# Kernel optimization log

Hardware: AMD Instinct MI355X
Metric: run time of the kernel (lower is better)

Reference implementation:

```python
import jax, jax.numpy as jnp
import numpy as np

B, L, D, H = 32768, 11, 32, 4
HD = D // H
VOCAB, NPOS, PE = 10000, 16, 16
EPS = 1e-5


def _safe_mask(m):
    # disable padding mask for rows where ALL positions are padding
    all_pad = m.all(axis=1)
    return m & ~all_pad[:, None]


def _aggregate(out, query_mask):
    sm = _safe_mask(query_mask)
    valid = (~sm)[..., None].astype(out.dtype)  # (B, L, 1)
    return (out * valid).sum(axis=1) / jnp.clip(valid.sum(axis=1), 1.0, None)


def _mha(xq, xkv, in_w, in_b, out_w, out_b, kpm):
    # torch nn.MultiheadAttention (batch_first, eval): packed in_proj then out_proj
    Bq, Lq, _ = xq.shape
    Wq, Wk, Wv = jnp.split(in_w, 3, axis=0)
    bq, bk, bv = jnp.split(in_b, 3, axis=0)
    q = (xq @ Wq.T + bq).reshape(Bq, Lq, H, HD)
    k = (xkv @ Wk.T + bk).reshape(Bq, -1, H, HD)
    v = (xkv @ Wv.T + bv).reshape(Bq, -1, H, HD)
    s = jnp.einsum('bqhd,bkhd->bhqk', q, k) / np.sqrt(HD).astype(np.float32)
    s = jnp.where(kpm[:, None, None, :], -jnp.inf, s)
    a = jax.nn.softmax(s, axis=-1)
    o = jnp.einsum('bhqk,bkhd->bqhd', a, v).reshape(Bq, Lq, D)
    return o @ out_w.T + out_b


def setup_inputs() -> dict:
    key = jax.random.key(0)
    ks = jax.random.split(key, 14)
    inp = {
        'home_players': jax.random.randint(ks[0], (B, L), 0, VOCAB),
        'away_players': jax.random.randint(ks[1], (B, L), 0, VOCAB),
        'h_positions': jax.random.randint(ks[2], (B, L), 0, NPOS),
        'a_positions': jax.random.randint(ks[3], (B, L), 0, NPOS),
        'emb': jax.random.normal(ks[4], (VOCAB, PE), jnp.float32) * 0.02,
        'pos_emb': jax.random.normal(ks[5], (NPOS, PE), jnp.float32) * 0.02,
        'h2a_in_w': jax.random.normal(ks[6], (3 * D, D), jnp.float32) * 0.05,
        'h2a_in_b': jnp.zeros((3 * D,), jnp.float32),
        'h2a_out_w': jax.random.normal(ks[7], (D, D), jnp.float32) * 0.05,
        'h2a_out_b': jnp.zeros((D,), jnp.float32),
        'a2h_in_w': jax.random.normal(ks[8], (3 * D, D), jnp.float32) * 0.05,
        'a2h_in_b': jnp.zeros((3 * D,), jnp.float32),
        'a2h_out_w': jax.random.normal(ks[9], (D, D), jnp.float32) * 0.05,
        'a2h_out_b': jnp.zeros((D,), jnp.float32),
        'gate_w': jax.random.normal(ks[10], (D, 2 * D), jnp.float32) * 0.05,
        'gate_b': jnp.zeros((D,), jnp.float32),
        'ln_w': jnp.ones((D,), jnp.float32),
        'ln_b': jnp.zeros((D,), jnp.float32),
    }
    return inp


def reference(home_players, away_players, h_positions, a_positions,
              emb, pos_emb,
              h2a_in_w, h2a_in_b, h2a_out_w, h2a_out_b,
              a2h_in_w, a2h_in_b, a2h_out_w, a2h_out_b,
              gate_w, gate_b, ln_w, ln_b):
    h_vecs = jnp.concatenate([emb[home_players], pos_emb[h_positions]], axis=-1)  # (B,L,D)
    a_vecs = jnp.concatenate([emb[away_players], pos_emb[a_positions]], axis=-1)
    h_mask = home_players == 0
    a_mask = away_players == 0
    h2a_out = _mha(h_vecs, a_vecs, h2a_in_w, h2a_in_b, h2a_out_w, h2a_out_b, _safe_mask(a_mask))
    h2a_vec = _aggregate(h2a_out, h_mask)
    a2h_out = _mha(a_vecs, h_vecs, a2h_in_w, a2h_in_b, a2h_out_w, a2h_out_b, _safe_mask(h_mask))
    a2h_vec = _aggregate(a2h_out, a_mask)
    concat = jnp.concatenate([h2a_vec, a2h_vec], axis=1)
    gate = jax.nn.sigmoid(concat @ gate_w.T + gate_b)
    matchup = gate * h2a_vec + (1.0 - gate) * a2h_vec
    mu = matchup.mean(axis=-1, keepdims=True)
    var = ((matchup - mu) ** 2).mean(axis=-1, keepdims=True)
    return (matchup - mu) / jnp.sqrt(var + EPS) * ln_w + ln_b
```

## Files before the change

### kernel.cpp

```cpp
#include <hip/hip_runtime.h>
#include <hip/hip_bf16.h>

typedef unsigned int u32;
typedef unsigned short u16;
typedef short bf16x8 __attribute__((ext_vector_type(8)));
typedef float f32x4 __attribute__((ext_vector_type(4)));

#define LQ 11
#define RPB 8
#define NR 88
#define PSTR 40
#define XSTR 32

__device__ __forceinline__ float blo(u32 x) { return __uint_as_float(x << 16); }
__device__ __forceinline__ float bhi(u32 x) { return __uint_as_float(x & 0xFFFF0000u); }
__device__ __forceinline__ float bf1(u16 x) { return __uint_as_float(((u32)x) << 16); }
__device__ __forceinline__ u16 f2b(float f) {
    __hip_bfloat16 h = __float2bfloat16(f);
    return *reinterpret_cast<u16*>(&h);
}
__device__ __forceinline__ u32 pk2(float a, float b) {
    return (u32)f2b(a) | ((u32)f2b(b) << 16);
}

__global__ __launch_bounds__(512, 6)
void CrossTeam_v7(const int* __restrict__ home, const int* __restrict__ away,
                  const int* __restrict__ hpos, const int* __restrict__ apos,
                  const float* __restrict__ emb, const float* __restrict__ pemb,
                  const float* __restrict__ h2a_w, const float* __restrict__ h2a_b,
                  const float* __restrict__ h2a_ow, const float* __restrict__ h2a_ob,
                  const float* __restrict__ a2h_w, const float* __restrict__ a2h_b,
                  const float* __restrict__ a2h_ow, const float* __restrict__ a2h_ob,
                  const float* __restrict__ gw, const float* __restrict__ gb,
                  const float* __restrict__ lnw, const float* __restrict__ lnb,
                  float* __restrict__ out)
{
    __shared__ u16 proj[6][NR * PSTR];
    __shared__ union {
        u16 xst[2][NR * XSTR];
        struct {
            float obuf[2][RPB][32];
            float ybuf[2][RPB][32];
        } cd;
    } u;
    __shared__ u32 mraw[2][RPB];

    const int t = threadIdx.x;
    const int b0 = blockIdx.x * RPB;

    if (t < 192) {
        const int side = t / 96;
        const int s = t - side * 96;
        if (s < NR) {
            const int r = s / 11, l = s - r * 11;
            const int gi = (b0 + r) * LQ + l;
            const int pid = side ? away[gi] : home[gi];
            const int pp  = side ? apos[gi] : hpos[gi];
            const f32x4* er = (const f32x4*)(emb + pid * 16);
            const f32x4* pr = (const f32x4*)(pemb + pp * 16);
            const f32x4 e0 = er[0], e1 = er[1], e2 = er[2], e3 = er[3];
            const f32x4 p0 = pr[0], p1 = pr[1], p2 = pr[2], p3 = pr[3];
            uint4 q0, q1, q2, q3;
            q0.x = pk2(e0[0], e0[1]); q0.y = pk2(e0[2], e0[3]);
            q0.z = pk2(e1[0], e1[1]); q0.w = pk2(e1[2], e1[3]);
            q1.x = pk2(e2[0], e2[1]); q1.y = pk2(e2[2], e2[3]);
            q1.z = pk2(e3[0], e3[1]); q1.w = pk2(e3[2], e3[3]);
            q2.x = pk2(p0[0], p0[1]); q2.y = pk2(p0[2], p0[3]);
            q2.z = pk2(p1[0], p1[1]); q2.w = pk2(p1[2], p1[3]);
            q3.x = pk2(p2[0], p2[1]); q3.y = pk2(p2[2], p2[3]);
            q3.z = pk2(p3[0], p3[1]); q3.w = pk2(p3[2], p3[3]);
            uint4* dst = (uint4*)&u.xst[side][s * XSTR];
            const int sw = s & 3;
            dst[0 ^ sw] = q0; dst[1 ^ sw] = q1; dst[2 ^ sw] = q2; dst[3 ^ sw] = q3;
        }
    }
    if (t >= 496) {
        const int k = t - 496; const int side = k >> 3; const int r = k & 7;
        const int* arr = side ? away : home;
        u32 m = 0;
        for (int l = 0; l < LQ; ++l) m |= (u32)(arr[(b0 + r) * LQ + l] == 0) << l;
        mraw[side][r] = m;
    }
    __syncthreads();

    const int wave = t >> 6, lane = t & 63;
    const int lq = lane >> 4, lm = lane & 15;

    {
        const int side = wave >> 2;
        const int mh = (wave >> 1) & 1;
        const int nh = wave & 1;
        const float* wq_src  = side ? a2h_w : h2a_w;
        const float* wkv_src = side ? h2a_w : a2h_w;
        const float* bq_src  = side ? a2h_b : h2a_b;
        const float* bkv_src = side ? h2a_b : a2h_b;
        bf16x8 afrag[3]; float bias[3][4];
        #pragma unroll
        for (int i = 0; i < 3; ++i) {
            const int M = (mh * 3 + i) * 16;
            const float* ws = (M < 32) ? wq_src : wkv_src;
            const float* wp = ws + (M + lm) * 32 + lq * 8;
            const f32x4 a0 = *(const f32x4*)wp;
            const f32x4 a1 = *(const f32x4*)(wp + 4);
            union { bf16x8 v; u32 w[4]; } au;
            au.w[0] = pk2(a0[0], a0[1]); au.w[1] = pk2(a0[2], a0[3]);
            au.w[2] = pk2(a1[0], a1[1]); au.w[3] = pk2(a1[2], a1[3]);
            afrag[i] = au.v;
            const float* bs = (M < 32) ? bq_src : bkv_src;
            #pragma unroll
            for (int j = 0; j < 4; ++j) bias[i][j] = bs[M + lq * 4 + j];
        }
        #pragma unroll
        for (int nn = 0; nn < 3; ++nn) {
            const int n = nh * 3 + nn;
            const int row = n * 16 + lm;
            const int rrow = row < NR ? row : NR - 1;
            const bf16x8 bfrag = *(const bf16x8*)
                &u.xst[side][rrow * XSTR + ((lq ^ (rrow & 3)) * 8)];
            #pragma unroll
            for (int i = 0; i < 3; ++i) {
                f32x4 acc = { bias[i][0], bias[i][1], bias[i][2], bias[i][3] };
                acc = __builtin_amdgcn_mfma_f32_16x16x32_bf16(afrag[i], bfrag, acc, 0, 0, 0);
                const int mt = mh * 3 + i;
                const int mat = side * 3 + (mt >> 1);
                const int dimw = (mt & 1) * 16 + lq * 4;
                if (row < NR) {
                    uint2 pk;
                    pk.x = pk2(acc[0], acc[1]);
                    pk.y = pk2(acc[2], acc[3]);
                    *(uint2*)&proj[mat][row * PSTR + dimw] = pk;
                }
            }
        }
    }
    __syncthreads();

    {
        const int hh = lane >> 4;
        const int slot = lane & 15;
        const int qi = slot < 11 ? slot : 10;
        const int dpv = hh * 8 + (slot & 7);
        #pragma unroll
        for (int it = 0; it < 2; ++it) {
            const int task = wave * 2 + it;
            const int r = task >> 1, dir = task & 1;
            const int qmat = dir ? 3 : 0;
            const int kmat = dir ? 1 : 4;
            const int vmat = dir ? 2 : 5;
            const u32 kvraw = mraw[dir ? 0 : 1][r];
            const u32 kv = (kvraw == 0x7FFu) ? 0u : kvraw;
            const u32 qraw = mraw[dir ? 1 : 0][r];
            const u32 smq = (qraw == 0x7FFu) ? 0u : qraw;
            const u32 vm = (~smq) & 0x7FFu;
            const float invc = 1.0f / (float)__popc(vm);
            const float wqw = (slot < 11 && ((vm >> slot) & 1u)) ? invc : 0.f;
            const uint4 qp = *(const uint4*)&proj[qmat][(r * 11 + qi) * PSTR + hh * 8];
            float qv[8];
            qv[0]=blo(qp.x); qv[1]=bhi(qp.x); qv[2]=blo(qp.y); qv[3]=bhi(qp.y);
            qv[4]=blo(qp.z); qv[5]=bhi(qp.z); qv[6]=blo(qp.w); qv[7]=bhi(qp.w);
            float e[11]; float sum = 0.f;
            #pragma unroll
            for (int ki = 0; ki < 11; ++ki) {
                const uint4 kp = *(const uint4*)&proj[kmat][(r * 11 + ki) * PSTR + hh * 8];
                float s = qv[0]*blo(kp.x) + qv[1]*bhi(kp.x) + qv[2]*blo(kp.y) + qv[3]*bhi(kp.y)
                        + qv[4]*blo(kp.z) + qv[5]*bhi(kp.z) + qv[6]*blo(kp.w) + qv[7]*bhi(kp.w);
                s *= 0.35355339059327373f;
                e[ki] = ((kv >> ki) & 1u) ? 0.f : __expf(s);
                sum += e[ki];
            }
            const float rs = wqw / fmaxf(sum, 1e-20f);
            float o = 0.f;
            #pragma unroll
            for (int ki = 0; ki < 11; ++ki) {
                float v = e[ki] * rs;
                v += __shfl_xor(v, 1, 16);
                v += __shfl_xor(v, 2, 16);
                v += __shfl_xor(v, 4, 16);
                v += __shfl_xor(v, 8, 16);
                o += v * bf1(proj[vmat][(r * 11 + ki) * PSTR + dpv]);
            }
            if (slot < 8) u.cd.obuf[dir][r][dpv] = o;
        }
    }
    __syncthreads();

    if (t < 256) {
        const int r = t >> 5, d = t & 31;
        float yh = h2a_ob[d];
        const float* wr = h2a_ow + d * 32;
        #pragma unroll
        for (int c = 0; c < 32; ++c) yh += u.cd.obuf[0][r][c] * wr[c];
        float ya = a2h_ob[d];
        wr = a2h_ow + d * 32;
        #pragma unroll
        for (int c = 0; c < 32; ++c) ya += u.cd.obuf[1][r][c] * wr[c];
        u.cd.ybuf[0][r][d] = yh; u.cd.ybuf[1][r][d] = ya;
        float acc = gb[d];
        const float* gr = gw + d * 64;
        #pragma unroll
        for (int c = 0; c < 32; ++c) acc += u.cd.ybuf[0][r][c] * gr[c];
        #pragma unroll
        for (int c = 0; c < 32; ++c) acc += u.cd.ybuf[1][r][c] * gr[32 + c];
        const float g = 1.0f / (1.0f + __expf(-acc));
        const float m = g * yh + (1.0f - g) * ya;
        float s1 = m, s2 = m * m;
        #pragma unroll
        for (int off = 1; off < 32; off <<= 1) {
            s1 += __shfl_xor(s1, off, 32);
            s2 += __shfl_xor(s2, off, 32);
        }
        const float mu = s1 * 0.03125f;
        const float var = fmaxf(s2 * 0.03125f - mu * mu, 0.f);
        const float res = (m - mu) * rsqrtf(var + 1e-5f) * lnw[d] + lnb[d];
        out[(b0 + r) * 32 + d] = res;
    }
}

extern "C" void kernel_launch(void* const* d_in, const int* in_sizes, int n_in,
                              void* d_out, int out_size, void* d_ws, size_t ws_size,
                              hipStream_t stream) {
    (void)in_sizes; (void)n_in; (void)d_ws; (void)ws_size; (void)out_size;
    CrossTeam_v7<<<32768 / RPB, 512, 0, stream>>>(
        (const int*)d_in[0], (const int*)d_in[1], (const int*)d_in[2], (const int*)d_in[3],
        (const float*)d_in[4], (const float*)d_in[5],
        (const float*)d_in[6], (const float*)d_in[7], (const float*)d_in[8], (const float*)d_in[9],
        (const float*)d_in[10], (const float*)d_in[11], (const float*)d_in[12], (const float*)d_in[13],
        (const float*)d_in[14], (const float*)d_in[15], (const float*)d_in[16], (const float*)d_in[17],
        (float*)d_out);
}
```

Before: 190.4 us.

## Gather embeddings directly into MFMA fragments and swizzle projection LDS layout

Instead of staging bf16 embedding rows in shared memory, the kernel now stores only player and position ids in LDS, and each MMA lane gathers its B-fragment straight from the global embedding tables. The projection buffer drops its padded stride of 40 for a dense stride of 32 with an XOR swizzle to avoid bank conflicts, which shrinks LDS use. Launch bounds are raised to allow 8 blocks per CU. The trade-off is redundant global gathers across waves (each row's fragment is loaded by two waves) and a higher register pressure cap.

```diff
diff --git a/kernel.cpp b/kernel.cpp
--- a/kernel.cpp
+++ b/kernel.cpp
@@ -9,8 +9,6 @@
 #define LQ 11
 #define RPB 8
 #define NR 88
-#define PSTR 40
-#define XSTR 32
 
 __device__ __forceinline__ float blo(u32 x) { return __uint_as_float(x << 16); }
 __device__ __forceinline__ float bhi(u32 x) { return __uint_as_float(x & 0xFFFF0000u); }
@@ -23,8 +21,8 @@
     return (u32)f2b(a) | ((u32)f2b(b) << 16);
 }
 
-__global__ __launch_bounds__(512, 6)
-void CrossTeam_v7(const int* __restrict__ home, const int* __restrict__ away,
+__global__ __launch_bounds__(512, 8)
+void CrossTeam_v8(const int* __restrict__ home, const int* __restrict__ away,
                   const int* __restrict__ hpos, const int* __restrict__ apos,
                   const float* __restrict__ emb, const float* __restrict__ pemb,
                   const float* __restrict__ h2a_w, const float* __restrict__ h2a_b,
@@ -35,9 +33,9 @@
                   const float* __restrict__ lnw, const float* __restrict__ lnb,
                   float* __restrict__ out)
 {
-    __shared__ u16 proj[6][NR * PSTR];
+    __shared__ u16 proj[6][NR * 32];
     __shared__ union {
-        u16 xst[2][NR * XSTR];
+        int ptab[2][NR][2];
         struct {
             float obuf[2][RPB][32];
             float ybuf[2][RPB][32];
@@ -48,31 +46,13 @@
     const int t = threadIdx.x;
     const int b0 = blockIdx.x * RPB;
 
-    if (t < 192) {
-        const int side = t / 96;
-        const int s = t - side * 96;
-        if (s < NR) {
-            const int r = s / 11, l = s - r * 11;
-            const int gi = (b0 + r) * LQ + l;
-            const int pid = side ? away[gi] : home[gi];
-            const int pp  = side ? apos[gi] : hpos[gi];
-            const f32x4* er = (const f32x4*)(emb + pid * 16);
-            const f32x4* pr = (const f32x4*)(pemb + pp * 16);
-            const f32x4 e0 = er[0], e1 = er[1], e2 = er[2], e3 = er[3];
-            const f32x4 p0 = pr[0], p1 = pr[1], p2 = pr[2], p3 = pr[3];
-            uint4 q0, q1, q2, q3;
-            q0.x = pk2(e0[0], e0[1]); q0.y = pk2(e0[2], e0[3]);
-            q0.z = pk2(e1[0], e1[1]); q0.w = pk2(e1[2], e1[3]);
-            q1.x = pk2(e2[0], e2[1]); q1.y = pk2(e2[2], e2[3]);
-            q1.z = pk2(e3[0], e3[1]); q1.w = pk2(e3[2], e3[3]);
-            q2.x = pk2(p0[0], p0[1]); q2.y = pk2(p0[2], p0[3]);
-            q2.z = pk2(p1[0], p1[1]); q2.w = pk2(p1[2], p1[3]);
-            q3.x = pk2(p2[0], p2[1]); q3.y = pk2(p2[2], p2[3]);
-            q3.z = pk2(p3[0], p3[1]); q3.w = pk2(p3[2], p3[3]);
-            uint4* dst = (uint4*)&u.xst[side][s * XSTR];
-            const int sw = s & 3;
-            dst[0 ^ sw] = q0; dst[1 ^ sw] = q1; dst[2 ^ sw] = q2; dst[3 ^ sw] = q3;
-        }
+    if (t < 176) {
+        const int side = t / 88;
+        const int s = t - side * 88;
+        const int r = s / 11, l = s - r * 11;
+        const int gi = (b0 + r) * LQ + l;
+        u.ptab[side][s][0] = side ? away[gi] : home[gi];
+        u.ptab[side][s][1] = side ? apos[gi] : hpos[gi];
     }
     if (t >= 496) {
         const int k = t - 496; const int side = k >> 3; const int r = k & 7;
@@ -110,25 +90,36 @@
             #pragma unroll
             for (int j = 0; j < 4; ++j) bias[i][j] = bs[M + lq * 4 + j];
         }
+        bf16x8 bfrag[3];
         #pragma unroll
         for (int nn = 0; nn < 3; ++nn) {
-            const int n = nh * 3 + nn;
-            const int row = n * 16 + lm;
-            const int rrow = row < NR ? row : NR - 1;
-            const bf16x8 bfrag = *(const bf16x8*)
-                &u.xst[side][rrow * XSTR + ((lq ^ (rrow & 3)) * 8)];
+            const int srow = (nh * 3 + nn) * 16 + lm;
+            const int s = srow < NR ? srow : NR - 1;
+            const int id = u.ptab[side][s][lq >> 1];
+            const float* gp = ((lq < 2) ? emb : pemb) + id * 16 + (lq & 1) * 8;
+            const f32x4 g0 = *(const f32x4*)gp;
+            const f32x4 g1 = *(const f32x4*)(gp + 4);
+            union { bf16x8 v; u32 w[4]; } bu;
+            bu.w[0] = pk2(g0[0], g0[1]); bu.w[1] = pk2(g0[2], g0[3]);
+            bu.w[2] = pk2(g1[0], g1[1]); bu.w[3] = pk2(g1[2], g1[3]);
+            bfrag[nn] = bu.v;
+        }
+        #pragma unroll
+        for (int nn = 0; nn < 3; ++nn) {
+            const int srow = (nh * 3 + nn) * 16 + lm;
             #pragma unroll
             for (int i = 0; i < 3; ++i) {
                 f32x4 acc = { bias[i][0], bias[i][1], bias[i][2], bias[i][3] };
-                acc = __builtin_amdgcn_mfma_f32_16x16x32_bf16(afrag[i], bfrag, acc, 0, 0, 0);
+                acc = __builtin_amdgcn_mfma_f32_16x16x32_bf16(afrag[i], bfrag[nn], acc, 0, 0, 0);
                 const int mt = mh * 3 + i;
                 const int mat = side * 3 + (mt >> 1);
                 const int dimw = (mt & 1) * 16 + lq * 4;
-                if (row < NR) {
+                if (srow < NR) {
+                    const int phys = srow * 32 + ((((dimw >> 3) ^ srow) & 3) << 3) + (dimw & 7);
                     uint2 pk;
                     pk.x = pk2(acc[0], acc[1]);
                     pk.y = pk2(acc[2], acc[3]);
-                    *(uint2*)&proj[mat][row * PSTR + dimw] = pk;
+                    *(uint2*)&proj[mat][phys] = pk;
                 }
             }
         }
@@ -147,6 +138,7 @@
             const int qmat = dir ? 3 : 0;
             const int kmat = dir ? 1 : 4;
             const int vmat = dir ? 2 : 5;
+            const int r11 = r * 11;
             const u32 kvraw = mraw[dir ? 0 : 1][r];
             const u32 kv = (kvraw == 0x7FFu) ? 0u : kvraw;
             const u32 qraw = mraw[dir ? 1 : 0][r];
@@ -154,14 +146,16 @@
             const u32 vm = (~smq) & 0x7FFu;
             const float invc = 1.0f / (float)__popc(vm);
             const float wqw = (slot < 11 && ((vm >> slot) & 1u)) ? invc : 0.f;
-            const uint4 qp = *(const uint4*)&proj[qmat][(r * 11 + qi) * PSTR + hh * 8];
+            const int qrow = r11 + qi;
+            const uint4 qp = *(const uint4*)&proj[qmat][qrow * 32 + (((hh ^ qrow) & 3) << 3)];
             float qv[8];
             qv[0]=blo(qp.x); qv[1]=bhi(qp.x); qv[2]=blo(qp.y); qv[3]=bhi(qp.y);
             qv[4]=blo(qp.z); qv[5]=bhi(qp.z); qv[6]=blo(qp.w); qv[7]=bhi(qp.w);
             float e[11]; float sum = 0.f;
             #pragma unroll
             for (int ki = 0; ki < 11; ++ki) {
-                const uint4 kp = *(const uint4*)&proj[kmat][(r * 11 + ki) * PSTR + hh * 8];
+                const int krow = r11 + ki;
+                const uint4 kp = *(const uint4*)&proj[kmat][krow * 32 + (((hh ^ krow) & 3) << 3)];
                 float s = qv[0]*blo(kp.x) + qv[1]*bhi(kp.x) + qv[2]*blo(kp.y) + qv[3]*bhi(kp.y)
                         + qv[4]*blo(kp.z) + qv[5]*bhi(kp.z) + qv[6]*blo(kp.w) + qv[7]*bhi(kp.w);
                 s *= 0.35355339059327373f;
@@ -177,7 +171,9 @@
                 v += __shfl_xor(v, 2, 16);
                 v += __shfl_xor(v, 4, 16);
                 v += __shfl_xor(v, 8, 16);
-                o += v * bf1(proj[vmat][(r * 11 + ki) * PSTR + dpv]);
+                const int vrow = r11 + ki;
+                const float vv = bf1(proj[vmat][vrow * 32 + (((hh ^ vrow) & 3) << 3) + (slot & 7)]);
+                o += v * vv;
             }
             if (slot < 8) u.cd.obuf[dir][r][dpv] = o;
         }
@@ -220,7 +216,7 @@
                               void* d_out, int out_size, void* d_ws, size_t ws_size,
                               hipStream_t stream) {
     (void)in_sizes; (void)n_in; (void)d_ws; (void)ws_size; (void)out_size;
-    CrossTeam_v7<<<32768 / RPB, 512, 0, stream>>>(
+    CrossTeam_v8<<<32768 / RPB, 512, 0, stream>>>(
         (const int*)d_in[0], (const int*)d_in[1], (const int*)d_in[2], (const int*)d_in[3],
         (const float*)d_in[4], (const float*)d_in[5],
         (const float*)d_in[6], (const float*)d_in[7], (const float*)d_in[8], (const float*)d_in[9],
```

New measurement: 207.9 us. 1.09x slower.
